# Kernel optimization log

Hardware: AMD Instinct MI355X
Metric: run time of the kernel (lower is better)

Reference implementation:

```python
import jax, jax.numpy as jnp
import numpy as np
import math

NUM_HEADS = 12
EMBED_DIM = 768

def setup_inputs() -> dict:
    key = jax.random.key(0)
    ks = jax.random.split(key, 9)
    B, T, D = 2, 2048, EMBED_DIM
    s = 1.0 / math.sqrt(D)
    inp = {
        "x": jax.random.normal(ks[0], (B, T, D), dtype=jnp.float32),
        "Wq": jax.random.normal(ks[1], (D, D), dtype=jnp.float32) * s,
        "bq": jnp.zeros((D,), dtype=jnp.float32),
        "Wk": jax.random.normal(ks[2], (D, D), dtype=jnp.float32) * s,
        "bk": jnp.zeros((D,), dtype=jnp.float32),
        "Wv": jax.random.normal(ks[3], (D, D), dtype=jnp.float32) * s,
        "bv": jnp.zeros((D,), dtype=jnp.float32),
        "Wo": jax.random.normal(ks[4], (D, D), dtype=jnp.float32) * s,
        "bo": jnp.zeros((D,), dtype=jnp.float32),
    }
    return inp

def reference(x, Wq, bq, Wk, bk, Wv, bv, Wo, bo):
    B, T, D = x.shape
    H = NUM_HEADS
    Dh = D // H
    # QKV projections, split heads: [B, H, T, Dh]
    def proj(W, b):
        y = x @ W.T + b
        return y.reshape(B, T, H, Dh).transpose(0, 2, 1, 3)
    q = proj(Wq, bq)
    k = proj(Wk, bk)
    v = proj(Wv, bv)
    scores = jnp.einsum('bhtd,bhsd->bhts', q, k) / math.sqrt(Dh)  # [B,H,T,T]
    attn = jax.nn.softmax(scores, axis=-1)
    ctx = jnp.einsum('bhts,bhsd->bhtd', attn, v)  # [B,H,T,Dh]
    ctx = ctx.transpose(0, 2, 1, 3).reshape(B, T, D)
    out = ctx @ Wo.T + bo
    return out
```

## Files before the change

### kernel.cpp

```cpp
#include <hip/hip_runtime.h>
#include <math.h>

using f32x4   = __attribute__((ext_vector_type(4))) float;
using bf16x8  = __attribute__((ext_vector_type(8))) short;

constexpr int Bb = 2;
constexpr int T  = 2048;
constexpr int D  = 768;
constexpr int H  = 12;
constexpr int Dh = 64;
constexpr int M  = Bb * T;
constexpr int NQKV = 3 * D;
#define SCALE_Q 0.18033688011112042f

__device__ __forceinline__ unsigned short f2bf(float f) {
    unsigned u = __float_as_uint(f);
    u += 0x7fffu + ((u >> 16) & 1u);
    return (unsigned short)(u >> 16);
}

__device__ __forceinline__ ushort4 f2bf4(float4 f) {
    return make_ushort4(f2bf(f.x), f2bf(f.y), f2bf(f.z), f2bf(f.w));
}

__device__ __forceinline__ void async_copy16(const void* g, void* lds_base) {
    __builtin_amdgcn_global_load_lds(
        (const __attribute__((address_space(1))) unsigned int*)g,
        (__attribute__((address_space(3))) unsigned int*)lds_base, 16, 0, 0);
}

__global__ __launch_bounds__(256) void prep_kernel(
    const float4* __restrict__ x,
    const float4* __restrict__ Wq, const float4* __restrict__ Wk,
    const float4* __restrict__ Wv, const float4* __restrict__ Wo,
    const float* __restrict__ bq, const float* __restrict__ bk, const float* __restrict__ bv,
    ushort4* __restrict__ Xb, ushort4* __restrict__ Wqkvb, ushort4* __restrict__ Wob,
    float* __restrict__ biasS)
{
    const int stride = gridDim.x * 256;
    const int i0 = blockIdx.x * 256 + threadIdx.x;
    const int NX = M * D / 4;
    const int NW = D * D / 4;
    for (int i = i0; i < NX; i += stride) Xb[i] = f2bf4(x[i]);
    for (int i = i0; i < NW; i += stride) {
        Wqkvb[i]          = f2bf4(Wq[i]);
        Wqkvb[NW + i]     = f2bf4(Wk[i]);
        Wqkvb[2 * NW + i] = f2bf4(Wv[i]);
        Wob[i]            = f2bf4(Wo[i]);
    }
    for (int i = i0; i < D; i += stride) {
        biasS[i]         = bq[i];
        biasS[D + i]     = bk[i];
        biasS[2 * D + i] = bv[i];
    }
}

template <int MODE, int TM>
__global__ __launch_bounds__(256) void gemm_bt_kernel(
    const unsigned short* __restrict__ A, const unsigned short* __restrict__ Bm,
    const float* __restrict__ bias, const int Kdim, const int Ndim,
    float* __restrict__ Cout,
    unsigned short* __restrict__ Qo, unsigned short* __restrict__ Ko,
    unsigned short* __restrict__ Vo)
{
    constexpr int IW = TM / 32;
    __shared__ unsigned short As[TM * 32];
    __shared__ unsigned short Bs[128 * 32];
    const int tid  = threadIdx.x;
    const int lane = tid & 63, wv = tid >> 6;
    const int l15  = lane & 15, l4 = lane >> 4;
    const int wr   = wv >> 1,  wc = wv & 1;

    const int lin = blockIdx.y * gridDim.x + blockIdx.x;
    const int gx  = (lin >> 3) % gridDim.x;
    const int gy  = (lin / (8 * gridDim.x)) * 8 + (lin & 7);
    const int row0 = gy * TM, col0 = gx * 128;

    f32x4 acc[IW][4];
    #pragma unroll
    for (int i = 0; i < IW; ++i)
        #pragma unroll
        for (int j = 0; j < 4; ++j)
            acc[i][j] = (f32x4){0.f, 0.f, 0.f, 0.f};

    for (int k0 = 0; k0 < Kdim; k0 += 32) {
        __syncthreads();
        #pragma unroll
        for (int i = 0; i < IW / 2; ++i) {
            const int offb = (wv * (IW / 2) + i) * 1024;
            const int off  = offb + lane * 16;
            const int r = off >> 6, cb = (off & 63) >> 1;
            async_copy16(A + (size_t)(row0 + r) * Kdim + k0 + cb, (char*)As + offb);
        }
        #pragma unroll
        for (int i = 0; i < 2; ++i) {
            const int offb = (wv * 2 + i) * 1024;
            const int off  = offb + lane * 16;
            const int r = off >> 6, cb = (off & 63) >> 1;
            async_copy16(Bm + (size_t)(col0 + r) * Kdim + k0 + cb, (char*)Bs + offb);
        }
        __syncthreads();

        bf16x8 af[IW], bfr[4];
        #pragma unroll
        for (int i = 0; i < IW; ++i)
            af[i] = *(const bf16x8*)((const char*)As + (wr * (TM / 2) + i * 16 + l15) * 64 + l4 * 16);
        #pragma unroll
        for (int j = 0; j < 4; ++j)
            bfr[j] = *(const bf16x8*)((const char*)Bs + (wc * 64 + j * 16 + l15) * 64 + l4 * 16);
        #pragma unroll
        for (int i = 0; i < IW; ++i)
            #pragma unroll
            for (int j = 0; j < 4; ++j)
                acc[i][j] = __builtin_amdgcn_mfma_f32_16x16x32_bf16(af[i], bfr[j], acc[i][j], 0, 0, 0);
    }

    if (MODE == 0) {
        #pragma unroll
        for (int j = 0; j < 4; ++j) {
            const int n = col0 + wc * 64 + j * 16 + l15;
            const float bv_ = bias[n];
            #pragma unroll
            for (int i = 0; i < IW; ++i) {
                #pragma unroll
                for (int r = 0; r < 4; ++r) {
                    const int m = row0 + wr * (TM / 2) + i * 16 + l4 * 4 + r;
                    Cout[(size_t)m * Ndim + n] = acc[i][j][r] + bv_;
                }
            }
        }
    } else {
        #pragma unroll
        for (int j = 0; j < 4; ++j) {
            const int n = col0 + wc * 64 + j * 16 + l15;
            const int which = n / D;
            const int hd = n % D;
            const int h = hd >> 6, d = hd & 63;
            const float bv_ = bias[n];
            if (which == 2) {
                #pragma unroll
                for (int i = 0; i < IW; ++i) {
                    const int m0 = row0 + wr * (TM / 2) + i * 16 + l4 * 4;
                    const int b = m0 >> 11, t = m0 & (T - 1);
                    float4 v4;
                    v4.x = acc[i][j][0] + bv_; v4.y = acc[i][j][1] + bv_;
                    v4.z = acc[i][j][2] + bv_; v4.w = acc[i][j][3] + bv_;
                    *(ushort4*)&Vo[((size_t)(b * H + h) * Dh + d) * T + t] = f2bf4(v4);
                }
            } else {
                const float scale = (which == 0) ? SCALE_Q : 1.0f;
                unsigned short* dst = (which == 0) ? Qo : Ko;
                #pragma unroll
                for (int i = 0; i < IW; ++i) {
                    #pragma unroll
                    for (int r = 0; r < 4; ++r) {
                        const int m = row0 + wr * (TM / 2) + i * 16 + l4 * 4 + r;
                        const int b = m >> 11, t = m & (T - 1);
                        dst[((size_t)(b * H + h) * T + t) * Dh + d] =
                            f2bf((acc[i][j][r] + bv_) * scale);
                    }
                }
            }
        }
    }
}

__global__ __launch_bounds__(256) void attn_kernel(
    const unsigned short* __restrict__ Q, const unsigned short* __restrict__ Kg,
    const unsigned short* __restrict__ Vt, unsigned short* __restrict__ Ctx)
{
    __shared__ unsigned short Ks[2][64 * 64];
    __shared__ unsigned short Vs[2][64 * 64];
    __shared__ unsigned short Ps[64 * 64];
    const int bh = blockIdx.y;
    const int q0 = blockIdx.x * 64;
    const int tid = threadIdx.x, lane = tid & 63, wv = tid >> 6;
    const int l15 = lane & 15, l4 = lane >> 4;
    const unsigned short* Qp = Q  + (size_t)bh * T * Dh;
    const unsigned short* Kp = Kg + (size_t)bh * T * Dh;
    const unsigned short* Vp = Vt + (size_t)bh * Dh * T;

    bf16x8 qf[2];
    #pragma unroll
    for (int ks = 0; ks < 2; ++ks)
        qf[ks] = *(const bf16x8*)&Qp[(size_t)(q0 + wv * 16 + l15) * Dh + ks * 32 + l4 * 8];

    const short oneb = (short)0x3F80;
    const bf16x8 onesf = {oneb, oneb, oneb, oneb, oneb, oneb, oneb, oneb};

    auto load_tiles = [&](int kt, int buf) {
        #pragma unroll
        for (int i = 0; i < 2; ++i) {
            const int offb = wv * 2048 + i * 1024;
            const int off  = offb + lane * 16;
            const int r = off >> 7;
            const int blk = (off & 127) >> 4;
            const int gc = (blk ^ (r & 7)) << 3;
            async_copy16(Kp + (size_t)(kt + r) * Dh + gc, (char*)&Ks[buf][0] + offb);
            async_copy16(Vp + (size_t)r * T + kt + gc,    (char*)&Vs[buf][0] + offb);
        }
    };

    load_tiles(0, 0);
    f32x4 o[4], oL;
    #pragma unroll
    for (int nj = 0; nj < 4; ++nj) o[nj] = (f32x4){0.f, 0.f, 0.f, 0.f};
    oL = (f32x4){0.f, 0.f, 0.f, 0.f};

    for (int kt64 = 0; kt64 < T / 64; ++kt64) {
        const int cur = kt64 & 1;
        __syncthreads();
        if (kt64 + 1 < T / 64) load_tiles((kt64 + 1) * 64, cur ^ 1);

        f32x4 s[4];
        #pragma unroll
        for (int nj = 0; nj < 4; ++nj) s[nj] = (f32x4){0.f, 0.f, 0.f, 0.f};
        #pragma unroll
        for (int ks = 0; ks < 2; ++ks) {
            #pragma unroll
            for (int nj = 0; nj < 4; ++nj) {
                bf16x8 kb = *(const bf16x8*)((const char*)&Ks[cur][0] +
                        (nj * 16 + l15) * 128 + (((ks << 2) + l4) ^ (l15 & 7)) * 16);
                s[nj] = __builtin_amdgcn_mfma_f32_16x16x32_bf16(qf[ks], kb, s[nj], 0, 0, 0);
            }
        }

        #pragma unroll
        for (int nj = 0; nj < 4; ++nj) {
            #pragma unroll
            for (int r = 0; r < 4; ++r) {
                const float p = __builtin_amdgcn_exp2f(fminf(s[nj][r], 80.0f));
                const int row = wv * 16 + l4 * 4 + r;
                const int blk = (nj * 2 + (l15 >> 3)) ^ (row & 7);
                *(unsigned short*)((char*)Ps + row * 128 + blk * 16 + (l15 & 7) * 2) =
                    (unsigned short)(__float_as_uint(p) >> 16);
            }
        }

        #pragma unroll
        for (int ks = 0; ks < 2; ++ks) {
            bf16x8 pa = *(const bf16x8*)((const char*)Ps +
                    (wv * 16 + l15) * 128 + (((ks << 2) + l4) ^ (l15 & 7)) * 16);
            oL = __builtin_amdgcn_mfma_f32_16x16x32_bf16(pa, onesf, oL, 0, 0, 0);
            #pragma unroll
            for (int nj = 0; nj < 4; ++nj) {
                bf16x8 vb = *(const bf16x8*)((const char*)&Vs[cur][0] +
                        (nj * 16 + l15) * 128 + (((ks << 2) + l4) ^ (l15 & 7)) * 16);
                o[nj] = __builtin_amdgcn_mfma_f32_16x16x32_bf16(pa, vb, o[nj], 0, 0, 0);
            }
        }
    }

    const int b = bh / H, h = bh % H;
    #pragma unroll
    for (int r = 0; r < 4; ++r) {
        const float inv = 1.0f / oL[r];
        const int t = q0 + wv * 16 + l4 * 4 + r;
        #pragma unroll
        for (int nj = 0; nj < 4; ++nj) {
            const int col = h * 64 + nj * 16 + l15;
            Ctx[(size_t)(b * T + t) * D + col] = f2bf(o[nj][r] * inv);
        }
    }
}

extern "C" void kernel_launch(void* const* d_in, const int* in_sizes, int n_in,
                              void* d_out, int out_size, void* d_ws, size_t ws_size,
                              hipStream_t stream) {
    const float* x  = (const float*)d_in[0];
    const float* Wq = (const float*)d_in[1];
    const float* bq = (const float*)d_in[2];
    const float* Wk = (const float*)d_in[3];
    const float* bk = (const float*)d_in[4];
    const float* Wv = (const float*)d_in[5];
    const float* bv = (const float*)d_in[6];
    const float* Wo = (const float*)d_in[7];
    const float* bo = (const float*)d_in[8];
    float* out = (float*)d_out;

    char* w = (char*)d_ws;
    auto alloc = [&](size_t bytes) {
        char* p = w; w += (bytes + 255) & ~(size_t)255; return p;
    };
    unsigned short* Xb    = (unsigned short*)alloc((size_t)M * D * 2);
    unsigned short* Wqkvb = (unsigned short*)alloc((size_t)NQKV * D * 2);
    unsigned short* Wob   = (unsigned short*)alloc((size_t)D * D * 2);
    float*          biasS = (float*)alloc((size_t)NQKV * 4);
    unsigned short* Qb    = (unsigned short*)alloc((size_t)M * D * 2);
    unsigned short* Kb    = (unsigned short*)alloc((size_t)M * D * 2);
    unsigned short* Vtb   = (unsigned short*)alloc((size_t)M * D * 2);
    unsigned short* Ctxb  = (unsigned short*)alloc((size_t)M * D * 2);

    prep_kernel<<<1024, 256, 0, stream>>>(
        (const float4*)x, (const float4*)Wq, (const float4*)Wk, (const float4*)Wv,
        (const float4*)Wo, bq, bk, bv,
        (ushort4*)Xb, (ushort4*)Wqkvb, (ushort4*)Wob, biasS);

    gemm_bt_kernel<1, 128><<<dim3(NQKV / 128, M / 128), 256, 0, stream>>>(
        Xb, Wqkvb, biasS, D, NQKV, nullptr, Qb, Kb, Vtb);

    attn_kernel<<<dim3(T / 64, Bb * H), 256, 0, stream>>>(Qb, Kb, Vtb, Ctxb);

    gemm_bt_kernel<0, 64><<<dim3(D / 128, M / 64), 256, 0, stream>>>(
        Ctxb, Wob, bo, D, D, out, nullptr, nullptr, nullptr);
}
```

Measured before the change: 181.3 us.

## Keep attention probabilities in registers via transposed QK^T and permuted V layout

The score MFMA is computed transposed (K as A operand, Q as B operand), so each lane's accumulator outputs can be packed directly into the bf16 A-operand fragment for the PV MFMA. This removes the LDS round trip for the P tile (the scattered 2-byte stores, the reads and the shared buffer). To make this work, the QKV GEMM epilogue writes V^T with a permuted token order that matches the register layout. P is now rounded to nearest-even instead of truncated, which adds a few ALU ops per element.

```diff
diff --git a/kernel.cpp b/kernel.cpp
--- a/kernel.cpp
+++ b/kernel.cpp
@@ -21,6 +21,13 @@
 
 __device__ __forceinline__ ushort4 f2bf4(float4 f) {
     return make_ushort4(f2bf(f.x), f2bf(f.y), f2bf(f.z), f2bf(f.w));
+}
+
+__device__ __forceinline__ unsigned rnepk(float a, float b) {
+    unsigned ua = __float_as_uint(a), ub = __float_as_uint(b);
+    ua += 0x7fffu + ((ua >> 16) & 1u);
+    ub += 0x7fffu + ((ub >> 16) & 1u);
+    return (ub & 0xffff0000u) | (ua >> 16);
 }
 
 __device__ __forceinline__ void async_copy16(const void* g, void* lds_base) {
@@ -142,10 +149,12 @@
                 for (int i = 0; i < IW; ++i) {
                     const int m0 = row0 + wr * (TM / 2) + i * 16 + l4 * 4;
                     const int b = m0 >> 11, t = m0 & (T - 1);
+                    const int g = (t >> 2) & 3, h16 = (t >> 4) & 1;
+                    const int tp = (t & ~31) | (g << 3) | (h16 << 2);
                     float4 v4;
                     v4.x = acc[i][j][0] + bv_; v4.y = acc[i][j][1] + bv_;
                     v4.z = acc[i][j][2] + bv_; v4.w = acc[i][j][3] + bv_;
-                    *(ushort4*)&Vo[((size_t)(b * H + h) * Dh + d) * T + t] = f2bf4(v4);
+                    *(ushort4*)&Vo[((size_t)(b * H + h) * Dh + d) * T + tp] = f2bf4(v4);
                 }
             } else {
                 const float scale = (which == 0) ? SCALE_Q : 1.0f;
@@ -171,7 +180,6 @@
 {
     __shared__ unsigned short Ks[2][64 * 64];
     __shared__ unsigned short Vs[2][64 * 64];
-    __shared__ unsigned short Ps[64 * 64];
     const int bh = blockIdx.y;
     const int q0 = blockIdx.x * 64;
     const int tid = threadIdx.x, lane = tid & 63, wv = tid >> 6;
@@ -182,8 +190,8 @@
 
     bf16x8 qf[2];
     #pragma unroll
-    for (int ks = 0; ks < 2; ++ks)
-        qf[ks] = *(const bf16x8*)&Qp[(size_t)(q0 + wv * 16 + l15) * Dh + ks * 32 + l4 * 8];
+    for (int c = 0; c < 2; ++c)
+        qf[c] = *(const bf16x8*)&Qp[(size_t)(q0 + wv * 16 + l15) * Dh + c * 32 + l4 * 8];
 
     const short oneb = (short)0x3F80;
     const bf16x8 onesf = {oneb, oneb, oneb, oneb, oneb, oneb, oneb, oneb};
@@ -212,41 +220,40 @@
         __syncthreads();
         if (kt64 + 1 < T / 64) load_tiles((kt64 + 1) * 64, cur ^ 1);
 
-        f32x4 s[4];
-        #pragma unroll
-        for (int nj = 0; nj < 4; ++nj) s[nj] = (f32x4){0.f, 0.f, 0.f, 0.f};
-        #pragma unroll
-        for (int ks = 0; ks < 2; ++ks) {
+        f32x4 St[4];
+        #pragma unroll
+        for (int k16 = 0; k16 < 4; ++k16) St[k16] = (f32x4){0.f, 0.f, 0.f, 0.f};
+        #pragma unroll
+        for (int c = 0; c < 2; ++c) {
+            #pragma unroll
+            for (int k16 = 0; k16 < 4; ++k16) {
+                const int row = k16 * 16 + l15;
+                bf16x8 kb = *(const bf16x8*)((const char*)&Ks[cur][0] +
+                        row * 128 + ((((c << 2) + l4)) ^ (row & 7)) * 16);
+                St[k16] = __builtin_amdgcn_mfma_f32_16x16x32_bf16(kb, qf[c], St[k16], 0, 0, 0);
+            }
+        }
+
+        #pragma unroll
+        for (int k16 = 0; k16 < 4; ++k16)
+            #pragma unroll
+            for (int r = 0; r < 4; ++r)
+                St[k16][r] = __builtin_amdgcn_exp2f(fminf(St[k16][r], 80.0f));
+
+        #pragma unroll
+        for (int G = 0; G < 2; ++G) {
+            union { unsigned u[4]; bf16x8 v; } pu;
+            pu.u[0] = rnepk(St[2 * G][0],     St[2 * G][1]);
+            pu.u[1] = rnepk(St[2 * G][2],     St[2 * G][3]);
+            pu.u[2] = rnepk(St[2 * G + 1][0], St[2 * G + 1][1]);
+            pu.u[3] = rnepk(St[2 * G + 1][2], St[2 * G + 1][3]);
+            oL = __builtin_amdgcn_mfma_f32_16x16x32_bf16(pu.v, onesf, oL, 0, 0, 0);
             #pragma unroll
             for (int nj = 0; nj < 4; ++nj) {
-                bf16x8 kb = *(const bf16x8*)((const char*)&Ks[cur][0] +
-                        (nj * 16 + l15) * 128 + (((ks << 2) + l4) ^ (l15 & 7)) * 16);
-                s[nj] = __builtin_amdgcn_mfma_f32_16x16x32_bf16(qf[ks], kb, s[nj], 0, 0, 0);
-            }
-        }
-
-        #pragma unroll
-        for (int nj = 0; nj < 4; ++nj) {
-            #pragma unroll
-            for (int r = 0; r < 4; ++r) {
-                const float p = __builtin_amdgcn_exp2f(fminf(s[nj][r], 80.0f));
-                const int row = wv * 16 + l4 * 4 + r;
-                const int blk = (nj * 2 + (l15 >> 3)) ^ (row & 7);
-                *(unsigned short*)((char*)Ps + row * 128 + blk * 16 + (l15 & 7) * 2) =
-                    (unsigned short)(__float_as_uint(p) >> 16);
-            }
-        }
-
-        #pragma unroll
-        for (int ks = 0; ks < 2; ++ks) {
-            bf16x8 pa = *(const bf16x8*)((const char*)Ps +
-                    (wv * 16 + l15) * 128 + (((ks << 2) + l4) ^ (l15 & 7)) * 16);
-            oL = __builtin_amdgcn_mfma_f32_16x16x32_bf16(pa, onesf, oL, 0, 0, 0);
-            #pragma unroll
-            for (int nj = 0; nj < 4; ++nj) {
+                const int row = nj * 16 + l15;
                 bf16x8 vb = *(const bf16x8*)((const char*)&Vs[cur][0] +
-                        (nj * 16 + l15) * 128 + (((ks << 2) + l4) ^ (l15 & 7)) * 16);
-                o[nj] = __builtin_amdgcn_mfma_f32_16x16x32_bf16(pa, vb, o[nj], 0, 0, 0);
+                        row * 128 + ((((G << 2) + l4)) ^ (row & 7)) * 16);
+                o[nj] = __builtin_amdgcn_mfma_f32_16x16x32_bf16(pu.v, vb, o[nj], 0, 0, 0);
             }
         }
     }
```

Result: faster. 177.2 us (-2.3%).
